# Performance work log

Measured on AMD Instinct MI355X. Metric: run time of the kernel, lower is better.

Reference implementation:

```python
import jax, jax.numpy as jnp
import numpy as np


def setup_inputs() -> dict:
    key = jax.random.key(0)
    kx, kw = jax.random.split(key)
    x = jax.random.normal(kx, (32, 128, 64, 64), dtype=jnp.float32)
    weights = jax.random.normal(kw, (256, 128, 3, 3), dtype=jnp.float32) * 0.05
    return {"x": x, "weights": weights}


def reference(x, weights):
    # Valid-padding, stride-1, no-bias 2D cross-correlation, identical math
    # to the nested-loop HandmadeConv2d (sum over in_ch, kH, kW per output pixel).
    return jax.lax.conv_general_dilated(
        x, weights,
        window_strides=(1, 1),
        padding="VALID",
        dimension_numbers=("NCHW", "OIHW", "NCHW"),
    )
```

## Files before the change

kernel.cpp:

```cpp
#include <hip/hip_runtime.h>
#include <hip/hip_bf16.h>

typedef unsigned short ushort;
typedef unsigned int uint;
typedef __bf16 bf16x8 __attribute__((ext_vector_type(8)));
typedef float f32x4 __attribute__((ext_vector_type(4)));
typedef uint uint4v __attribute__((ext_vector_type(4)));
typedef uint uint2v __attribute__((ext_vector_type(2)));

#define CI 128
#define HIN 64
#define WIN 64
#define CO 256
#define HO 62
#define WO 62
#define NB 32
#define KTOT 1152
#define PIXIMG 3844
#define NPIX 123008
#define XIMG 524288
#define NKT 18

__device__ __forceinline__ ushort f2bf(float f) {
  uint u = __builtin_bit_cast(uint, f);
  u += 0x7fffu + ((u >> 16) & 1u);
  return (ushort)(u >> 16);
}

__global__ void repack_w_kernel(const float* __restrict__ w, ushort* __restrict__ w2) {
  const int co = blockIdx.x;
  for (int idx = threadIdx.x; idx < KTOT; idx += 256) {
    const int t  = idx >> 7;
    const int ci = idx & 127;
    w2[co * KTOT + idx] = f2bf(w[(co * CI + ci) * 9 + t]);
  }
}

#define XPAD 132
__global__ __launch_bounds__(256) void repack_x_kernel(const float* __restrict__ x,
                                                       ushort* __restrict__ x2) {
  __shared__ float t[WIN * XPAD];
  const int n = blockIdx.y;
  const int h = blockIdx.x;
  const int tid = threadIdx.x;
  const float* src = x + ((size_t)n * CI * HIN + h) * WIN;
  #pragma unroll
  for (int it = 0; it < 8; ++it) {
    const int idx = it * 256 + tid;
    const int ci  = idx >> 4;
    const int w4  = (idx & 15) * 4;
    const float4 v = *reinterpret_cast<const float4*>(src + (size_t)ci * (HIN * WIN) + w4);
    t[(w4 + 0) * XPAD + ci] = v.x;
    t[(w4 + 1) * XPAD + ci] = v.y;
    t[(w4 + 2) * XPAD + ci] = v.z;
    t[(w4 + 3) * XPAD + ci] = v.w;
  }
  __syncthreads();
  ushort* dst = x2 + ((size_t)(n * HIN + h) * WIN) * CI;
  #pragma unroll
  for (int it = 0; it < 4; ++it) {
    const int idx = it * 256 + tid;
    const int w   = idx >> 4;
    const int cig = idx & 15;
    const float* p = &t[w * XPAD + cig * 8];
    uint4v q;
    q[0] = (uint)f2bf(p[0]) | ((uint)f2bf(p[1]) << 16);
    q[1] = (uint)f2bf(p[2]) | ((uint)f2bf(p[3]) << 16);
    q[2] = (uint)f2bf(p[4]) | ((uint)f2bf(p[5]) << 16);
    q[3] = (uint)f2bf(p[6]) | ((uint)f2bf(p[7]) << 16);
    *reinterpret_cast<uint4v*>(dst + (size_t)w * CI + cig * 8) = q;
  }
}


#define GLOAD(SRC, DSTOFF) \
  __builtin_amdgcn_global_load_lds( \
      (const __attribute__((address_space(1))) uint*)(const void*)(SRC), \
      (__attribute__((address_space(3))) uint*)(void*)&lds[DSTOFF], 16, 0, 0)

#define STAGE_A(DB, SLOT, KT) do { \
  const int _ca = (KT) * 64; \
  GLOAD(w2 + aOff[(SLOT) >> 1][0] + _ca, (DB) + (SLOT) * 8192 + stgu);       \
  GLOAD(w2 + aOff[(SLOT) >> 1][1] + _ca, (DB) + (SLOT) * 8192 + stgu + 512); \
} while (0)

#define STAGE_B(DB, SLOT, KT) do { \
  const int _tp = (KT) >> 1; \
  const int _rr = (_tp * 11) >> 5; \
  const int _cb = (_rr * WIN + (_tp - _rr * 3)) * CI + ((KT) & 1) * 64; \
  GLOAD(x2 + bOff[(SLOT) >> 1][0] + _cb, (DB) + (SLOT) * 8192 + stgu);       \
  GLOAD(x2 + bOff[(SLOT) >> 1][1] + _cb, (DB) + (SLOT) * 8192 + stgu + 512); \
} while (0)

#define LOAD_A(F0, F1, LDB, SLOT) do { \
  _Pragma("unroll") for (int mf = 0; mf < 4; ++mf) { \
    F0[mf] = *reinterpret_cast<const bf16x8*>(&lds[(LDB) + (SLOT) * 8192 + arow + mf * 1024 + ck0]); \
    F1[mf] = *reinterpret_cast<const bf16x8*>(&lds[(LDB) + (SLOT) * 8192 + arow + mf * 1024 + ck1]); } \
} while (0)

#define LOAD_B(F0, F1, LDB, SLOT) do { \
  _Pragma("unroll") for (int nf = 0; nf < 2; ++nf) { \
    F0[nf] = *reinterpret_cast<const bf16x8*>(&lds[(LDB) + (SLOT) * 8192 + brow + nf * 1024 + ck0]); \
    F1[nf] = *reinterpret_cast<const bf16x8*>(&lds[(LDB) + (SLOT) * 8192 + brow + nf * 1024 + ck1]); } \
} while (0)

#define MMA(MG, NG, FA0, FA1, FB0, FB1) do { \
  __builtin_amdgcn_s_barrier(); \
  asm volatile("s_waitcnt lgkmcnt(0)" ::: "memory"); \
  __builtin_amdgcn_s_setprio(1); \
  _Pragma("unroll") for (int mf = 0; mf < 4; ++mf) \
    _Pragma("unroll") for (int nf = 0; nf < 2; ++nf) { \
      acc[(MG) * 4 + mf][(NG) * 2 + nf] = __builtin_amdgcn_mfma_f32_16x16x32_bf16( \
          FA0[mf], FB0[nf], acc[(MG) * 4 + mf][(NG) * 2 + nf], 0, 0, 0); \
      acc[(MG) * 4 + mf][(NG) * 2 + nf] = __builtin_amdgcn_mfma_f32_16x16x32_bf16( \
          FA1[mf], FB1[nf], acc[(MG) * 4 + mf][(NG) * 2 + nf], 0, 0, 0); } \
  __builtin_amdgcn_s_setprio(0); \
  __builtin_amdgcn_s_barrier(); \
} while (0)

__global__ __launch_bounds__(512, 2)
void conv_8ph_kernel(const ushort* __restrict__ x2, const ushort* __restrict__ w2,
                     float* __restrict__ out)
{
  __shared__ alignas(16) ushort lds[65536];

  const int tid  = threadIdx.x;
  const int lane = tid & 63;
  const int wid  = tid >> 6;
  const int wm   = wid >> 2;
  const int wn   = wid & 3;

  const int p0 = blockIdx.x * 256;

  const int lrow = lane >> 3;
  const int lc   = (lane & 7) ^ lrow;
  const int stgu = wid * 1024;

  int aOff[2][2];
  #pragma unroll
  for (int h = 0; h < 2; ++h)
    #pragma unroll
    for (int j = 0; j < 2; ++j)
      aOff[h][j] = (h * 128 + wid * 16 + j * 8 + lrow) * KTOT + lc * 8;

  int bOff[2][2];
  #pragma unroll
  for (int h = 0; h < 2; ++h)
    #pragma unroll
    for (int j = 0; j < 2; ++j) {
      int pglob = p0 + h * 128 + wid * 16 + j * 8 + lrow;
      pglob = pglob < NPIX ? pglob : (NPIX - 1);
      const int nimg = pglob / PIXIMG;
      const int prem = pglob - nimg * PIXIMG;
      const int oh   = prem / WO;
      const int ow   = prem - oh * WO;
      bOff[h][j] = ((nimg * HIN + oh) * WIN + ow) * CI + lc * 8;
    }

  const int arow = (wm * 64 + (lane & 15)) * 64;
  const int brow = (wn * 32 + (lane & 15)) * 64;
  const int ck0  = ((lane >> 4) ^ (lane & 7)) * 8;
  const int ck1  = ((4 + (lane >> 4)) ^ (lane & 7)) * 8;

  f32x4 acc[8][4];
  #pragma unroll
  for (int i = 0; i < 8; ++i)
    #pragma unroll
    for (int j = 0; j < 4; ++j)
      acc[i][j] = (f32x4){0.f, 0.f, 0.f, 0.f};

  bf16x8 fa0k0[4], fa0k1[4], fa1k0[4], fa1k1[4];
  bf16x8 fb0k0[2], fb0k1[2], fb1k0[2], fb1k1[2];

  STAGE_B(0, 0, 0);
  STAGE_A(0, 1, 0);
  STAGE_B(0, 2, 0);
  STAGE_A(0, 3, 0);
  STAGE_B(32768, 0, 1);
  STAGE_A(32768, 1, 1);
  asm volatile("s_waitcnt vmcnt(4)" ::: "memory");
  __builtin_amdgcn_s_barrier();

  int ldb = 0;
  #pragma unroll 1
  for (int t = 0; t < 16; ++t) {
    LOAD_A(fa0k0, fa0k1, ldb, 1);
    LOAD_B(fb0k0, fb0k1, ldb, 0);
    STAGE_B(ldb ^ 32768, 2, t + 1);
    STAGE_A(ldb ^ 32768, 3, t + 1);
    MMA(0, 0, fa0k0, fa0k1, fb0k0, fb0k1);
    LOAD_A(fa1k0, fa1k1, ldb, 3);
    STAGE_B(ldb, 0, t + 2);
    STAGE_A(ldb, 1, t + 2);
    MMA(1, 0, fa1k0, fa1k1, fb0k0, fb0k1);
    LOAD_B(fb1k0, fb1k1, ldb, 2);
    MMA(0, 1, fa0k0, fa0k1, fb1k0, fb1k1);
    asm volatile("s_waitcnt vmcnt(4)" ::: "memory");
    MMA(1, 1, fa1k0, fa1k1, fb1k0, fb1k1);
    ldb ^= 32768;
  }
  LOAD_A(fa0k0, fa0k1, ldb, 1);
  LOAD_B(fb0k0, fb0k1, ldb, 0);
  STAGE_B(ldb ^ 32768, 2, 17);
  STAGE_A(ldb ^ 32768, 3, 17);
  MMA(0, 0, fa0k0, fa0k1, fb0k0, fb0k1);
  LOAD_A(fa1k0, fa1k1, ldb, 3);
  MMA(1, 0, fa1k0, fa1k1, fb0k0, fb0k1);
  LOAD_B(fb1k0, fb1k1, ldb, 2);
  MMA(0, 1, fa0k0, fa0k1, fb1k0, fb1k1);
  asm volatile("s_waitcnt vmcnt(0)" ::: "memory");
  MMA(1, 1, fa1k0, fa1k1, fb1k0, fb1k1);
  ldb ^= 32768;
  LOAD_A(fa0k0, fa0k1, ldb, 1);
  LOAD_B(fb0k0, fb0k1, ldb, 0);
  MMA(0, 0, fa0k0, fa0k1, fb0k0, fb0k1);
  LOAD_A(fa1k0, fa1k1, ldb, 3);
  MMA(1, 0, fa1k0, fa1k1, fb0k0, fb0k1);
  LOAD_B(fb1k0, fb1k1, ldb, 2);
  MMA(0, 1, fa0k0, fa0k1, fb1k0, fb1k1);
  MMA(1, 1, fa1k0, fa1k1, fb1k0, fb1k1);

  #pragma unroll
  for (int ni = 0; ni < 4; ++ni) {
    const int pix = p0 + (ni >> 1) * 128 + wn * 32 + (ni & 1) * 16 + (lane & 15);
    if (pix < NPIX) {
      const int n2  = pix / PIXIMG;
      const int pr2 = pix - n2 * PIXIMG;
      float* ob = out + (size_t)n2 * (CO * PIXIMG) + pr2;
      #pragma unroll
      for (int mi = 0; mi < 8; ++mi) {
        const int cobase = (mi >> 2) * 128 + wm * 64 + (mi & 3) * 16 + ((lane >> 4) * 4);
        float* po = ob + (size_t)cobase * PIXIMG;
        #pragma unroll
        for (int r = 0; r < 4; ++r)
          po[(size_t)r * PIXIMG] = acc[mi][ni][r];
      }
    }
  }
}

__global__ __launch_bounds__(256, 3)
void conv_fallback_kernel(const float* __restrict__ x, const float* __restrict__ wt,
                          float* __restrict__ out)
{
  __shared__ alignas(16) ushort a_lds[128 * 64];
  __shared__ alignas(16) ushort b_lds[128 * 64];

  const int tid  = threadIdx.x;
  const int lane = tid & 63;
  const int wid  = tid >> 6;
  const int wrow = wid >> 1;
  const int wcol = wid & 1;
  const int co0 = blockIdx.x * 128;
  const int p0  = blockIdx.y * 128;

  const int pl    = tid & 127;
  const int kgsel = __builtin_amdgcn_readfirstlane(tid >> 7);
  const int pglob = p0 + pl;
  const int nimg  = pglob / PIXIMG;
  const int prem  = pglob - nimg * PIXIMG;
  const int oh    = prem / WO;
  const int ow    = prem - oh * WO;
  const int xpix  = nimg * XIMG + oh * WIN + ow;

  const int frow_a = wrow * 64 + (lane & 15);
  const int frow_b = wcol * 64 + (lane & 15);
  int aoff[2], boff[2];
  #pragma unroll
  for (int kk = 0; kk < 2; ++kk) {
    const int chk = (kk * 4 + (lane >> 4)) ^ (lane & 7);
    aoff[kk] = frow_a * 64 + chk * 8;
    boff[kk] = frow_b * 64 + chk * 8;
  }

  f32x4 acc[4][4];
  #pragma unroll
  for (int i = 0; i < 4; ++i)
    #pragma unroll
    for (int j = 0; j < 4; ++j)
      acc[i][j] = (f32x4){0.f, 0.f, 0.f, 0.f};

  for (int kt = 0; kt < NKT; ++kt) {
    const int k0 = kt * 64;
    if (kt) __syncthreads();

    #pragma unroll
    for (int it = 0; it < 4; ++it) {
      const int kg = kgsel + it * 2;
      uint pk[4];
      #pragma unroll
      for (int j = 0; j < 8; ++j) {
        const int k  = k0 + kg * 8 + j;
        const int ci = k / 9;
        const int rs = k - ci * 9;
        const int r  = rs / 3;
        const int s  = rs - r * 3;
        const ushort u = f2bf(x[xpix + ci * (HIN * WIN) + r * WIN + s]);
        if (j & 1) pk[j >> 1] |= ((uint)u) << 16;
        else       pk[j >> 1]  = (uint)u;
      }
      uint4v q = {pk[0], pk[1], pk[2], pk[3]};
      *reinterpret_cast<uint4v*>(&b_lds[pl * 64 + ((kg ^ (pl & 7)) * 8)]) = q;
    }

    #pragma unroll
    for (int i = 0; i < 8; ++i) {
      const int id  = i * 256 + tid;
      const int row = id >> 4;
      const int c4  = id & 15;
      const float4 v = *reinterpret_cast<const float4*>(
          wt + (size_t)(co0 + row) * KTOT + k0 + c4 * 4);
      uint2v q;
      q[0] = (uint)f2bf(v.x) | ((uint)f2bf(v.y) << 16);
      q[1] = (uint)f2bf(v.z) | ((uint)f2bf(v.w) << 16);
      *reinterpret_cast<uint2v*>(
          &a_lds[row * 64 + (((c4 >> 1) ^ (row & 7)) * 8) + (c4 & 1) * 4]) = q;
    }

    __syncthreads();

    #pragma unroll
    for (int kk = 0; kk < 2; ++kk) {
      bf16x8 af[4], bb[4];
      #pragma unroll
      for (int mi = 0; mi < 4; ++mi)
        af[mi] = *reinterpret_cast<const bf16x8*>(&a_lds[aoff[kk] + mi * (16 * 64)]);
      #pragma unroll
      for (int ni = 0; ni < 4; ++ni)
        bb[ni] = *reinterpret_cast<const bf16x8*>(&b_lds[boff[kk] + ni * (16 * 64)]);
      #pragma unroll
      for (int mi = 0; mi < 4; ++mi)
        #pragma unroll
        for (int ni = 0; ni < 4; ++ni)
          acc[mi][ni] = __builtin_amdgcn_mfma_f32_16x16x32_bf16(af[mi], bb[ni], acc[mi][ni], 0, 0, 0);
    }
  }

  #pragma unroll
  for (int ni = 0; ni < 4; ++ni) {
    const int pix = p0 + wcol * 64 + ni * 16 + (lane & 15);
    const int n2  = pix / PIXIMG;
    const int pr2 = pix - n2 * PIXIMG;
    float* ob = out + (size_t)n2 * (CO * PIXIMG) + pr2
                    + (size_t)(co0 + wrow * 64 + ((lane >> 4) * 4)) * PIXIMG;
    #pragma unroll
    for (int mi = 0; mi < 4; ++mi) {
      float* po = ob + (size_t)mi * (16 * PIXIMG);
      #pragma unroll
      for (int r = 0; r < 4; ++r)
        po[(size_t)r * PIXIMG] = acc[mi][ni][r];
    }
  }
}

extern "C" void kernel_launch(void* const* d_in, const int* in_sizes, int n_in,
                              void* d_out, int out_size, void* d_ws, size_t ws_size,
                              hipStream_t stream) {
  const float* x  = (const float*)d_in[0];
  const float* wt = (const float*)d_in[1];
  float* out = (float*)d_out;

  ushort* w2 = (ushort*)d_ws;
  ushort* x2 = (ushort*)((char*)d_ws + 589824);

  const size_t need = 589824 + (size_t)NB * XIMG * 2;

  if (ws_size >= need) {
    repack_w_kernel<<<dim3(CO), dim3(256), 0, stream>>>(wt, w2);
    repack_x_kernel<<<dim3(HIN, NB), dim3(256), 0, stream>>>(x, x2);
    conv_8ph_kernel<<<dim3(481), dim3(512), 0, stream>>>(x2, w2, out);
  } else {
    conv_fallback_kernel<<<dim3(CO / 128, NPIX / 128), dim3(256), 0, stream>>>(x, wt, out);
  }
}
```

Measured before the change: 113.9 us.

## Software-pipeline LDS fragment loads across k-tiles and drop explicit lgkmcnt waits

Restructures the main loop so the LDS fragment loads for the next k-tile are issued during the MFMA phases of the current tile. It uses extra register buffers and a 2x unrolled loop with ping-pong fragment sets, and redistributes the global staging loads and vmcnt waits between the quadrants. It also removes the explicit lgkmcnt(0) wait inside each MMA block and relies on compiler-inserted waits. This is meant to hide LDS latency behind matrix work, at the cost of higher VGPR pressure under 512-thread, 2-block launch bounds, which could cause spills. The barrier placement relative to LDS reads of slots being restaged also becomes more delicate.

```diff
diff --git a/kernel.cpp b/kernel.cpp
--- a/kernel.cpp
+++ b/kernel.cpp
@@ -104,18 +104,36 @@
     F1[nf] = *reinterpret_cast<const bf16x8*>(&lds[(LDB) + (SLOT) * 8192 + brow + nf * 1024 + ck1]); } \
 } while (0)
 
-#define MMA(MG, NG, FA0, FA1, FB0, FB1) do { \
+#define VMW4 asm volatile("s_waitcnt vmcnt(4)" ::: "memory")
+
+#define MMAQ(MG, NG, A0, A1, B0, B1) do { \
   __builtin_amdgcn_s_barrier(); \
-  asm volatile("s_waitcnt lgkmcnt(0)" ::: "memory"); \
   __builtin_amdgcn_s_setprio(1); \
   _Pragma("unroll") for (int mf = 0; mf < 4; ++mf) \
     _Pragma("unroll") for (int nf = 0; nf < 2; ++nf) { \
       acc[(MG) * 4 + mf][(NG) * 2 + nf] = __builtin_amdgcn_mfma_f32_16x16x32_bf16( \
-          FA0[mf], FB0[nf], acc[(MG) * 4 + mf][(NG) * 2 + nf], 0, 0, 0); \
+          A0[mf], B0[nf], acc[(MG) * 4 + mf][(NG) * 2 + nf], 0, 0, 0); \
       acc[(MG) * 4 + mf][(NG) * 2 + nf] = __builtin_amdgcn_mfma_f32_16x16x32_bf16( \
-          FA1[mf], FB1[nf], acc[(MG) * 4 + mf][(NG) * 2 + nf], 0, 0, 0); } \
+          A1[mf], B1[nf], acc[(MG) * 4 + mf][(NG) * 2 + nf], 0, 0, 0); } \
   __builtin_amdgcn_s_setprio(0); \
   __builtin_amdgcn_s_barrier(); \
+} while (0)
+
+#define TILE(LDB, FA0, FA1, FB0, FB1, NFA0, NFA1, NFB0, NFB1, TN1, TN2) do { \
+  LOAD_A(gaB0, gaB1, (LDB), 3);            \
+  STAGE_B((LDB) ^ 32768, 2, (TN1)); \
+  MMAQ(0, 0, FA0, FA1, FB0, FB1); \
+  LOAD_B(gbB0, gbB1, (LDB), 2);            \
+  STAGE_A((LDB) ^ 32768, 3, (TN1)); \
+  VMW4; \
+  MMAQ(1, 0, gaB0, gaB1, FB0, FB1); \
+  LOAD_A(NFA0, NFA1, (LDB) ^ 32768, 1);    \
+  STAGE_B((LDB), 0, (TN2)); \
+  MMAQ(0, 1, FA0, FA1, gbB0, gbB1); \
+  LOAD_B(NFB0, NFB1, (LDB) ^ 32768, 0);    \
+  STAGE_A((LDB), 1, (TN2)); \
+  VMW4; \
+  MMAQ(1, 1, gaB0, gaB1, gbB0, gbB1); \
 } while (0)
 
 __global__ __launch_bounds__(512, 2)
@@ -169,8 +187,8 @@
     for (int j = 0; j < 4; ++j)
       acc[i][j] = (f32x4){0.f, 0.f, 0.f, 0.f};
 
-  bf16x8 fa0k0[4], fa0k1[4], fa1k0[4], fa1k1[4];
-  bf16x8 fb0k0[2], fb0k1[2], fb1k0[2], fb1k1[2];
+  bf16x8 fA0[4], fA1[4], nA0[4], nA1[4], gaB0[4], gaB1[4];
+  bf16x8 fB0[2], fB1[2], nB0[2], nB1[2], gbB0[2], gbB1[2];
 
   STAGE_B(0, 0, 0);
   STAGE_A(0, 1, 0);
@@ -178,47 +196,37 @@
   STAGE_A(0, 3, 0);
   STAGE_B(32768, 0, 1);
   STAGE_A(32768, 1, 1);
-  asm volatile("s_waitcnt vmcnt(4)" ::: "memory");
+  VMW4;
   __builtin_amdgcn_s_barrier();
-
-  int ldb = 0;
+  LOAD_A(fA0, fA1, 0, 1);
+  LOAD_B(fB0, fB1, 0, 0);
+
   #pragma unroll 1
-  for (int t = 0; t < 16; ++t) {
-    LOAD_A(fa0k0, fa0k1, ldb, 1);
-    LOAD_B(fb0k0, fb0k1, ldb, 0);
-    STAGE_B(ldb ^ 32768, 2, t + 1);
-    STAGE_A(ldb ^ 32768, 3, t + 1);
-    MMA(0, 0, fa0k0, fa0k1, fb0k0, fb0k1);
-    LOAD_A(fa1k0, fa1k1, ldb, 3);
-    STAGE_B(ldb, 0, t + 2);
-    STAGE_A(ldb, 1, t + 2);
-    MMA(1, 0, fa1k0, fa1k1, fb0k0, fb0k1);
-    LOAD_B(fb1k0, fb1k1, ldb, 2);
-    MMA(0, 1, fa0k0, fa0k1, fb1k0, fb1k1);
-    asm volatile("s_waitcnt vmcnt(4)" ::: "memory");
-    MMA(1, 1, fa1k0, fa1k1, fb1k0, fb1k1);
-    ldb ^= 32768;
-  }
-  LOAD_A(fa0k0, fa0k1, ldb, 1);
-  LOAD_B(fb0k0, fb0k1, ldb, 0);
-  STAGE_B(ldb ^ 32768, 2, 17);
-  STAGE_A(ldb ^ 32768, 3, 17);
-  MMA(0, 0, fa0k0, fa0k1, fb0k0, fb0k1);
-  LOAD_A(fa1k0, fa1k1, ldb, 3);
-  MMA(1, 0, fa1k0, fa1k1, fb0k0, fb0k1);
-  LOAD_B(fb1k0, fb1k1, ldb, 2);
-  MMA(0, 1, fa0k0, fa0k1, fb1k0, fb1k1);
+  for (int i = 0; i < 8; ++i) {
+    const int t = 2 * i;
+    TILE(0,     fA0, fA1, fB0, fB1, nA0, nA1, nB0, nB1, t + 1, t + 2);
+    TILE(32768, nA0, nA1, nB0, nB1, fA0, fA1, fB0, fB1, t + 2, t + 3);
+  }
+
+  LOAD_A(gaB0, gaB1, 0, 3);
+  STAGE_B(32768, 2, 17);
+  MMAQ(0, 0, fA0, fA1, fB0, fB1);
+  LOAD_B(gbB0, gbB1, 0, 2);
+  STAGE_A(32768, 3, 17);
+  VMW4;
+  MMAQ(1, 0, gaB0, gaB1, fB0, fB1);
+  LOAD_A(nA0, nA1, 32768, 1);
+  MMAQ(0, 1, fA0, fA1, gbB0, gbB1);
+  LOAD_B(nB0, nB1, 32768, 0);
   asm volatile("s_waitcnt vmcnt(0)" ::: "memory");
-  MMA(1, 1, fa1k0, fa1k1, fb1k0, fb1k1);
-  ldb ^= 32768;
-  LOAD_A(fa0k0, fa0k1, ldb, 1);
-  LOAD_B(fb0k0, fb0k1, ldb, 0);
-  MMA(0, 0, fa0k0, fa0k1, fb0k0, fb0k1);
-  LOAD_A(fa1k0, fa1k1, ldb, 3);
-  MMA(1, 0, fa1k0, fa1k1, fb0k0, fb0k1);
-  LOAD_B(fb1k0, fb1k1, ldb, 2);
-  MMA(0, 1, fa0k0, fa0k1, fb1k0, fb1k1);
-  MMA(1, 1, fa1k0, fa1k1, fb1k0, fb1k1);
+  MMAQ(1, 1, gaB0, gaB1, gbB0, gbB1);
+
+  LOAD_A(gaB0, gaB1, 32768, 3);
+  MMAQ(0, 0, nA0, nA1, nB0, nB1);
+  LOAD_B(gbB0, gbB1, 32768, 2);
+  MMAQ(1, 0, gaB0, gaB1, nB0, nB1);
+  MMAQ(0, 1, nA0, nA1, gbB0, gbB1);
+  MMAQ(1, 1, gaB0, gaB1, gbB0, gbB1);
 
   #pragma unroll
   for (int ni = 0; ni < 4; ++ni) {
```

Result: slower. 342.9 us (+201.1%).
